# Performance work log

Hardware: AMD Instinct MI355X
Metric: run time of the kernel (lower is better)

## Reference

```python
import jax, jax.numpy as jnp
import numpy as np

H = 16          # num_heads
DK = 64         # k_dim_head
DV = 64         # v_dim_head
DIM = 1024      # model dim (= H*DK = H*DV)


def _split_heads(x, h):
    # ... T (H d) -> ... H T d
    x = x.reshape(x.shape[:-1] + (h, -1))
    return jnp.swapaxes(x, -2, -3)


def _merge_heads(x):
    # ... H T d -> ... T (H d)
    x = jnp.swapaxes(x, -2, -3)
    return x.reshape(x.shape[:-2] + (-1,))


def setup_inputs() -> dict:
    key = jax.random.key(0)
    ks = jax.random.split(key, 8)
    B, T = 2, 2048
    q = jax.random.normal(ks[0], (B, T, DIM), dtype=jnp.float32)
    k = jax.random.normal(ks[1], (B, T, DIM), dtype=jnp.float32)
    v = jax.random.normal(ks[2], (B, T, DIM), dtype=jnp.float32)
    # causal boolean mask [T, T] (True = attend)
    mask = jnp.tril(jnp.ones((T, T), dtype=bool))
    s = 1.0 / np.sqrt(DIM)
    # weights stored as [in, out] so projection is x @ W (== torch Linear, no bias)
    Wq = jax.random.normal(ks[3], (DIM, H * DK), dtype=jnp.float32) * s
    Wk = jax.random.normal(ks[4], (DIM, H * DK), dtype=jnp.float32) * s
    Wv = jax.random.normal(ks[5], (DIM, H * DV), dtype=jnp.float32) * s
    Wo = jax.random.normal(ks[6], (H * DV, DIM), dtype=jnp.float32) * s
    return {"q": q, "k": k, "v": v, "mask": mask,
            "Wq": Wq, "Wk": Wk, "Wv": Wv, "Wo": Wo}


def reference(q, k, v, mask, Wq, Wk, Wv, Wo):
    q_i = _split_heads(q @ Wq, H)                       # ... H T dk
    k_i = _split_heads(k @ Wk, H)                       # ... H T dk
    v_i = _split_heads(v @ Wv, H)                       # ... H T dv
    s_qk = jnp.einsum('...hik,...hjk->...hij', q_i, k_i) / jnp.sqrt(
        jnp.asarray(DK, dtype=q_i.dtype))               # ... H T T
    neg = -jnp.finfo(s_qk.dtype).max
    s_qk = jnp.where(mask, s_qk, neg)
    attn = jax.nn.softmax(s_qk, axis=-1)
    vals = jnp.einsum('...hij,...hjv->...hiv', attn, v_i)
    return _merge_heads(vals) @ Wo                      # ... T out_dim
```

## Files before the change

kernel.cpp:

```cpp
#include <hip/hip_runtime.h>
#include <hip/hip_bf16.h>
#include <stdint.h>

#define T_SEQ  2048
#define DMODEL 1024
#define NBATCH 2
#define NHEAD  16
#define DHEAD  64
#define MTOT   (NBATCH * T_SEQ)

typedef __attribute__((ext_vector_type(8))) short short8_t;
typedef __attribute__((ext_vector_type(4))) float f32x4;
typedef __attribute__((ext_vector_type(16))) float f32x16;
typedef __attribute__((ext_vector_type(2))) __bf16 bhalf2_t;
typedef __attribute__((ext_vector_type(4))) uint32_t uint4_t;

typedef const __attribute__((address_space(1))) void* gas_t;
typedef __attribute__((address_space(3))) void* las_t;

__device__ __forceinline__ ushort f2bf(float f) {
    return __builtin_bit_cast(unsigned short, (__bf16)f);
}
__device__ __forceinline__ uint32_t pk_bf16(float a, float b) {
    bhalf2_t t; t[0] = (__bf16)a; t[1] = (__bf16)b;
    return __builtin_bit_cast(uint32_t, t);
}

template <int B>
__device__ __forceinline__ short8_t pack8(const f32x16 &s) {
    uint4_t u;
    u[0] = pk_bf16(s[B + 0], s[B + 1]);
    u[1] = pk_bf16(s[B + 2], s[B + 3]);
    u[2] = pk_bf16(s[B + 4], s[B + 5]);
    u[3] = pk_bf16(s[B + 6], s[B + 7]);
    return __builtin_bit_cast(short8_t, u);
}

__global__ __launch_bounds__(256) void convert_qkv_kernel(
        const float* __restrict__ q, const float* __restrict__ k,
        const float* __restrict__ v, ushort* __restrict__ outb) {
    const size_t per = (size_t)MTOT * DMODEL / 4;
    size_t idx = (size_t)blockIdx.x * 256 + threadIdx.x;
    int t = (int)(idx / per);
    size_t i = idx - (size_t)t * per;
    const float4* src = (const float4*)(t == 0 ? q : (t == 1 ? k : v));
    float4 val = src[i];
    uint2 o;
    o.x = pk_bf16(val.x, val.y);
    o.y = pk_bf16(val.z, val.w);
    ((uint2*)outb)[(size_t)t * per + i] = o;
}

__global__ __launch_bounds__(256) void convw_kernel(
        const float* __restrict__ Wq, const float* __restrict__ Wk,
        const float* __restrict__ Wv, const float* __restrict__ Wo,
        ushort* __restrict__ wt) {
    __shared__ float tile[32][33];
    int z = blockIdx.z;
    const float* W = z == 0 ? Wq : z == 1 ? Wk : z == 2 ? Wv : Wo;
    const float sc = (z == 0) ? 0.18033688011f : 1.0f;
    ushort* out = wt + (size_t)z * DMODEL * DMODEL;
    int tx = threadIdx.x, ty = threadIdx.y;
    int k0 = blockIdx.x * 32, n0 = blockIdx.y * 32;
    #pragma unroll
    for (int i = 0; i < 4; i++)
        tile[ty + i * 8][tx] = W[(size_t)(k0 + ty + i * 8) * DMODEL + n0 + tx];
    __syncthreads();
    #pragma unroll
    for (int i = 0; i < 4; i++)
        out[(size_t)(n0 + ty + i * 8) * DMODEL + k0 + tx] = f2bf(tile[tx][ty + i * 8] * sc);
}

template <bool OUT_F32>
__global__ __launch_bounds__(256, 2) void gemm_bt_kernel(
        const ushort* __restrict__ Aall, const ushort* __restrict__ Btall,
        void* __restrict__ Call, int M, int N, int K) {
    const ushort* A  = Aall  + (size_t)blockIdx.z * M * K;
    const ushort* Bt = Btall + (size_t)blockIdx.z * N * K;

    __shared__ ushort As[128 * 32];
    __shared__ ushort Bs[128 * 32];

    const int tid  = threadIdx.x;
    const int lane = tid & 63;
    const int wid  = tid >> 6;
    const int wr = wid >> 1, wc = wid & 1;
    const int m_base = blockIdx.x * 128;
    const int n_base = blockIdx.y * 128;

    f32x4 acc[4][4] = {};

    const int srow = lane >> 2;
    const int scol = (lane & 3) * 8;

    for (int kk = 0; kk < K; kk += 32) {
        __syncthreads();
        #pragma unroll
        for (int i = 0; i < 2; i++) {
            int c = wid * 2 + i;
            const ushort* ga = A  + (size_t)(m_base + c * 16 + srow) * K + kk + scol;
            const ushort* gb = Bt + (size_t)(n_base + c * 16 + srow) * K + kk + scol;
            __builtin_amdgcn_global_load_lds((gas_t)ga, (las_t)(As + c * 512), 16, 0, 0);
            __builtin_amdgcn_global_load_lds((gas_t)gb, (las_t)(Bs + c * 512), 16, 0, 0);
        }
        __syncthreads();
        short8_t a[4], b[4];
        #pragma unroll
        for (int mt = 0; mt < 4; mt++)
            a[mt] = *(const short8_t*)(As + (wr * 64 + mt * 16 + (lane & 15)) * 32 + (lane >> 4) * 8);
        #pragma unroll
        for (int nt = 0; nt < 4; nt++)
            b[nt] = *(const short8_t*)(Bs + (wc * 64 + nt * 16 + (lane & 15)) * 32 + (lane >> 4) * 8);
        #pragma unroll
        for (int mt = 0; mt < 4; mt++)
            #pragma unroll
            for (int nt = 0; nt < 4; nt++)
                acc[mt][nt] = __builtin_amdgcn_mfma_f32_16x16x32_bf16(a[mt], b[nt], acc[mt][nt], 0, 0, 0);
    }

    const int row0 = m_base + wr * 64 + (lane >> 4) * 4;
    const int col0 = n_base + wc * 64 + (lane & 15);
    if constexpr (OUT_F32) {
        float* C = (float*)Call + (size_t)blockIdx.z * M * N;
        #pragma unroll
        for (int mt = 0; mt < 4; mt++)
            #pragma unroll
            for (int nt = 0; nt < 4; nt++)
                #pragma unroll
                for (int r = 0; r < 4; r++)
                    C[(size_t)(row0 + mt * 16 + r) * N + col0 + nt * 16] = acc[mt][nt][r];
    } else {
        ushort* C = (ushort*)Call + (size_t)blockIdx.z * M * N;
        #pragma unroll
        for (int mt = 0; mt < 4; mt++)
            #pragma unroll
            for (int nt = 0; nt < 4; nt++)
                #pragma unroll
                for (int r = 0; r < 4; r++)
                    C[(size_t)(row0 + mt * 16 + r) * N + col0 + nt * 16] = f2bf(acc[mt][nt][r]);
    }
}

__global__ __launch_bounds__(128, 2) void attn_kernel(
        const ushort* __restrict__ Qp, const ushort* __restrict__ Kp,
        const ushort* __restrict__ Vp, ushort* __restrict__ Op) {
    __shared__ __attribute__((aligned(16))) ushort Ksh[2][64 * 72];
    __shared__ __attribute__((aligned(16))) ushort Vts[2][64 * 72];

    const int tid = threadIdx.x, lane = tid & 63, w = tid >> 6;
    const int m31 = lane & 31, hi = lane >> 5;
    const int bh = blockIdx.y;
    const int b = bh >> 4, h = bh & 15;

    const ushort* Qb = Qp + (size_t)(b * T_SEQ) * DMODEL + h * DHEAD;
    const ushort* Kb = Kp + (size_t)(b * T_SEQ) * DMODEL + h * DHEAD;
    const ushort* Vb = Vp + (size_t)(b * T_SEQ) * DMODEL + h * DHEAD;
    ushort* Ob = Op + (size_t)(b * T_SEQ) * DMODEL + h * DHEAD;

    const int qi = 31 - (int)blockIdx.x;
    const int nt = qi + 1;
    const int q0 = qi * 64;
    const int q0w = q0 + w * 32;
    const int qg = q0w + m31;

    const int kr = tid >> 1, kc64 = (tid & 1) * 32;
    const int kvp = tid & 31, dvs = tid >> 5;
    const int lp = kvp & 7, q2 = lp >> 1;
    const int q2p = ((q2 & 1) << 1) | (q2 >> 1);
    const int kvc = (kvp & ~7) | (q2p << 1) | (lp & 1);

    short8_t kreg[4], vreg[4];
    auto LOADKV = [&](int kv0) {
        #pragma unroll
        for (int j = 0; j < 4; j++)
            kreg[j] = *(const short8_t*)(Kb + (size_t)(kv0 + kr) * DMODEL + kc64 + j * 8);
        const ushort* vsrc = Vb + (size_t)(kv0 + kvp * 2) * DMODEL + dvs * 16;
        vreg[0] = *(const short8_t*)(vsrc);
        vreg[1] = *(const short8_t*)(vsrc + 8);
        vreg[2] = *(const short8_t*)(vsrc + DMODEL);
        vreg[3] = *(const short8_t*)(vsrc + DMODEL + 8);
    };
    auto WRITEKV = [&](int buf) {
        #pragma unroll
        for (int j = 0; j < 4; j++)
            *(short8_t*)(&Ksh[buf][kr * 72 + kc64 + j * 8]) = kreg[j];
        #pragma unroll
        for (int c = 0; c < 2; c++) {
            uint4_t a = __builtin_bit_cast(uint4_t, vreg[c]);
            uint4_t o = __builtin_bit_cast(uint4_t, vreg[2 + c]);
            #pragma unroll
            for (int j = 0; j < 4; j++) {
                int d0 = dvs * 16 + c * 8 + 2 * j;
                *(uint32_t*)(&Vts[buf][(d0 + 0) * 72 + kvc * 2]) =
                    __builtin_amdgcn_perm(o[j], a[j], 0x05040100u);
                *(uint32_t*)(&Vts[buf][(d0 + 1) * 72 + kvc * 2]) =
                    __builtin_amdgcn_perm(o[j], a[j], 0x07060302u);
            }
        }
    };

    short8_t qf[4];
    #pragma unroll
    for (int dkc = 0; dkc < 4; dkc++)
        qf[dkc] = *(const short8_t*)(Qb + (size_t)(q0w + m31) * DMODEL + dkc * 16 + hi * 8);

    f32x16 acc0 = {}, acc1 = {};
    float mrun = -1e30f, lrun = 0.f;

    LOADKV(0);
    WRITEKV(0);
    LOADKV(64);

    for (int t = 0; t < nt; ++t) {
        const int kv0 = t * 64;
        const int cur = t & 1;
        const bool need_mask = (t == nt - 1);

        __syncthreads();
        if (t + 1 < nt) {
            WRITEKV(cur ^ 1);
            if (t + 2 < nt) LOADKV((t + 2) * 64);
        }

        f32x16 s0 = {}, s1 = {};
        __builtin_amdgcn_s_setprio(1);
        #pragma unroll
        for (int dkc = 0; dkc < 4; dkc++) {
            short8_t kf0 = *(const short8_t*)(&Ksh[cur][(m31) * 72 + dkc * 16 + hi * 8]);
            short8_t kf1 = *(const short8_t*)(&Ksh[cur][(32 + m31) * 72 + dkc * 16 + hi * 8]);
            s0 = __builtin_amdgcn_mfma_f32_32x32x16_bf16(kf0, qf[dkc], s0, 0, 0, 0);
            s1 = __builtin_amdgcn_mfma_f32_32x32x16_bf16(kf1, qf[dkc], s1, 0, 0, 0);
        }
        __builtin_amdgcn_s_setprio(0);

        if (need_mask) {
            const int kvb = kv0 + 4 * hi;
            #pragma unroll
            for (int r = 0; r < 16; r++) {
                int kvl = (r & 3) + 8 * (r >> 2);
                if (kvb + kvl      > qg) s0[r] = -1e30f;
                if (kvb + kvl + 32 > qg) s1[r] = -1e30f;
            }
        }

        float tm[16];
        #pragma unroll
        for (int r = 0; r < 16; r++) tm[r] = fmaxf(s0[r], s1[r]);
        #pragma unroll
        for (int st = 8; st >= 1; st >>= 1)
            #pragma unroll
            for (int i = 0; i < st; i++) tm[i] = fmaxf(tm[i], tm[i + st]);
        float pmax = fmaxf(tm[0], __shfl_xor(tm[0], 32));

        if (!__all(pmax <= mrun + 8.f)) {
            float mnew = fmaxf(mrun, pmax);
            float fac = exp2f(mrun - mnew);
            mrun = mnew;
            lrun *= fac;
            #pragma unroll
            for (int r = 0; r < 16; r++) {
                float fr = __shfl(fac, (r & 3) + 8 * (r >> 2) + 4 * hi);
                acc0[r] *= fr; acc1[r] *= fr;
            }
        }

        float ps[16];
        #pragma unroll
        for (int r = 0; r < 16; r++) {
            s0[r] = exp2f(s0[r] - mrun);
            s1[r] = exp2f(s1[r] - mrun);
            ps[r] = s0[r] + s1[r];
        }
        #pragma unroll
        for (int st = 8; st >= 1; st >>= 1)
            #pragma unroll
            for (int i = 0; i < st; i++) ps[i] += ps[i + st];
        lrun += ps[0] + __shfl_xor(ps[0], 32);

        short8_t pa[4];
        pa[0] = pack8<0>(s0);
        pa[1] = pack8<8>(s0);
        pa[2] = pack8<0>(s1);
        pa[3] = pack8<8>(s1);
        __builtin_amdgcn_s_setprio(1);
        #pragma unroll
        for (int ks = 0; ks < 4; ks++) {
            short8_t vf0 = *(const short8_t*)(&Vts[cur][(m31) * 72 + ks * 16 + hi * 8]);
            short8_t vf1 = *(const short8_t*)(&Vts[cur][(32 + m31) * 72 + ks * 16 + hi * 8]);
            acc0 = __builtin_amdgcn_mfma_f32_32x32x16_bf16(pa[ks], vf0, acc0, 0, 0, 0);
            acc1 = __builtin_amdgcn_mfma_f32_32x32x16_bf16(pa[ks], vf1, acc1, 0, 0, 0);
        }
        __builtin_amdgcn_s_setprio(0);
    }

    float linv = __builtin_amdgcn_rcpf(lrun);
    #pragma unroll
    for (int r = 0; r < 16; r++) {
        int ql = (r & 3) + 8 * (r >> 2) + 4 * hi;
        float li = __shfl(linv, ql);
        ushort* orow = Ob + (size_t)(q0w + ql) * DMODEL + m31;
        orow[0]  = f2bf(acc0[r] * li);
        orow[32] = f2bf(acc1[r] * li);
    }
}

extern "C" void kernel_launch(void* const* d_in, const int* in_sizes, int n_in,
                              void* d_out, int out_size, void* d_ws, size_t ws_size,
                              hipStream_t stream) {
    (void)in_sizes; (void)n_in; (void)out_size; (void)ws_size;
    const float* q  = (const float*)d_in[0];
    const float* k  = (const float*)d_in[1];
    const float* v  = (const float*)d_in[2];
    const float* Wq = (const float*)d_in[4];
    const float* Wk = (const float*)d_in[5];
    const float* Wv = (const float*)d_in[6];
    const float* Wo = (const float*)d_in[7];

    ushort* ws = (ushort*)d_ws;
    const size_t MK = (size_t)MTOT * DMODEL;
    const size_t NK = (size_t)DMODEL * DMODEL;
    ushort* qkvb = ws;
    ushort* wt   = ws + 3 * MK;
    ushort* qkvp = ws + 3 * MK + 4 * NK;
    ushort* Op   = ws;

    convert_qkv_kernel<<<dim3(12288), dim3(256), 0, stream>>>(q, k, v, qkvb);
    convw_kernel<<<dim3(32, 32, 4), dim3(32, 8), 0, stream>>>(Wq, Wk, Wv, Wo, wt);
    gemm_bt_kernel<false><<<dim3(32, 8, 3), dim3(256), 0, stream>>>(qkvb, wt, (void*)qkvp,
                                                                    MTOT, DMODEL, DMODEL);
    attn_kernel<<<dim3(32, 32), dim3(128), 0, stream>>>(qkvp, qkvp + MK, qkvp + 2 * MK, Op);
    gemm_bt_kernel<true><<<dim3(32, 8, 1), dim3(256), 0, stream>>>(Op, wt + 3 * NK, d_out,
                                                                   MTOT, DMODEL, DMODEL);
}
```

Before: 149.2 us.

## Schedule attention work units through a global atomic counter

The attention kernel now pulls work items from a global atomic counter, ordered longest-first (largest causal query tile first), instead of taking them from the fixed blockIdx mapping. A small kernel zeroes the counter before each launch. The aim is to balance the triangular causal workload across CUs so short tiles fill in behind long ones. The cost is an extra kernel launch plus two block barriers and an atomic per unit. The order also depends on the workspace having room for the counter.

New measurement: 149.3 us. Within noise of the previous version (+0.1%).

```diff
diff --git a/kernel.cpp b/kernel.cpp
--- a/kernel.cpp
+++ b/kernel.cpp
@@ -71,6 +71,10 @@
         out[(size_t)(n0 + ty + i * 8) * DMODEL + k0 + tx] = f2bf(tile[tx][ty + i * 8] * sc);
 }
 
+__global__ void zero_ctr_kernel(uint32_t* ctr) {
+    if (threadIdx.x == 0 && blockIdx.x == 0) *ctr = 0u;
+}
+
 template <bool OUT_F32>
 __global__ __launch_bounds__(256, 2) void gemm_bt_kernel(
         const ushort* __restrict__ Aall, const ushort* __restrict__ Btall,
@@ -143,25 +147,14 @@
 
 __global__ __launch_bounds__(128, 2) void attn_kernel(
         const ushort* __restrict__ Qp, const ushort* __restrict__ Kp,
-        const ushort* __restrict__ Vp, ushort* __restrict__ Op) {
+        const ushort* __restrict__ Vp, ushort* __restrict__ Op,
+        uint32_t* __restrict__ ctr) {
     __shared__ __attribute__((aligned(16))) ushort Ksh[2][64 * 72];
     __shared__ __attribute__((aligned(16))) ushort Vts[2][64 * 72];
+    __shared__ int unit_j;
 
     const int tid = threadIdx.x, lane = tid & 63, w = tid >> 6;
     const int m31 = lane & 31, hi = lane >> 5;
-    const int bh = blockIdx.y;
-    const int b = bh >> 4, h = bh & 15;
-
-    const ushort* Qb = Qp + (size_t)(b * T_SEQ) * DMODEL + h * DHEAD;
-    const ushort* Kb = Kp + (size_t)(b * T_SEQ) * DMODEL + h * DHEAD;
-    const ushort* Vb = Vp + (size_t)(b * T_SEQ) * DMODEL + h * DHEAD;
-    ushort* Ob = Op + (size_t)(b * T_SEQ) * DMODEL + h * DHEAD;
-
-    const int qi = 31 - (int)blockIdx.x;
-    const int nt = qi + 1;
-    const int q0 = qi * 64;
-    const int q0w = q0 + w * 32;
-    const int qg = q0w + m31;
 
     const int kr = tid >> 1, kc64 = (tid & 1) * 32;
     const int kvp = tid & 31, dvs = tid >> 5;
@@ -169,6 +162,8 @@
     const int q2p = ((q2 & 1) << 1) | (q2 >> 1);
     const int kvc = (kvp & ~7) | (q2p << 1) | (lp & 1);
 
+    const ushort *Qb, *Kb, *Vb;
+    ushort *Ob;
     short8_t kreg[4], vreg[4];
     auto LOADKV = [&](int kv0) {
         #pragma unroll
@@ -199,108 +194,128 @@
         }
     };
 
-    short8_t qf[4];
-    #pragma unroll
-    for (int dkc = 0; dkc < 4; dkc++)
-        qf[dkc] = *(const short8_t*)(Qb + (size_t)(q0w + m31) * DMODEL + dkc * 16 + hi * 8);
-
-    f32x16 acc0 = {}, acc1 = {};
-    float mrun = -1e30f, lrun = 0.f;
-
-    LOADKV(0);
-    WRITEKV(0);
-    LOADKV(64);
-
-    for (int t = 0; t < nt; ++t) {
-        const int kv0 = t * 64;
-        const int cur = t & 1;
-        const bool need_mask = (t == nt - 1);
-
+    for (;;) {
         __syncthreads();
-        if (t + 1 < nt) {
-            WRITEKV(cur ^ 1);
-            if (t + 2 < nt) LOADKV((t + 2) * 64);
+        if (tid == 0) unit_j = (int)atomicAdd(ctr, 1u);
+        __syncthreads();
+        const int j = unit_j;
+        if (j >= 1024) break;
+
+        const int u = 31 - (j >> 5);
+        const int bh = j & 31;
+        const int b = bh >> 4, h = bh & 15;
+        Qb = Qp + (size_t)(b * T_SEQ) * DMODEL + h * DHEAD;
+        Kb = Kp + (size_t)(b * T_SEQ) * DMODEL + h * DHEAD;
+        Vb = Vp + (size_t)(b * T_SEQ) * DMODEL + h * DHEAD;
+        Ob = Op + (size_t)(b * T_SEQ) * DMODEL + h * DHEAD;
+
+        const int nt = u + 1;
+        const int q0w = u * 64 + w * 32;
+        const int qg = q0w + m31;
+        const int diag = 2 * u + w;
+
+        short8_t qf[4];
+        #pragma unroll
+        for (int dkc = 0; dkc < 4; dkc++)
+            qf[dkc] = *(const short8_t*)(Qb + (size_t)(q0w + m31) * DMODEL + dkc * 16 + hi * 8);
+
+        f32x16 acc0 = {}, acc1 = {};
+        float mrun = -1e30f, lrun = 0.f;
+
+        LOADKV(0);
+        WRITEKV(0);
+        LOADKV(64);
+
+        for (int t = 0; t < nt; ++t) {
+            const int kv0 = t * 64;
+            const int cur = t & 1;
+            const bool need_mask = (t == nt - 1);
+
+            __syncthreads();
+            if (t + 1 < nt) {
+                WRITEKV(cur ^ 1);
+                if (t + 2 < nt) LOADKV((t + 2) * 64);
+            }
+
+            f32x16 s0 = {}, s1 = {};
+            __builtin_amdgcn_s_setprio(1);
+            #pragma unroll
+            for (int dkc = 0; dkc < 4; dkc++) {
+                short8_t kf0 = *(const short8_t*)(&Ksh[cur][(m31) * 72 + dkc * 16 + hi * 8]);
+                short8_t kf1 = *(const short8_t*)(&Ksh[cur][(32 + m31) * 72 + dkc * 16 + hi * 8]);
+                s0 = __builtin_amdgcn_mfma_f32_32x32x16_bf16(kf0, qf[dkc], s0, 0, 0, 0);
+                s1 = __builtin_amdgcn_mfma_f32_32x32x16_bf16(kf1, qf[dkc], s1, 0, 0, 0);
+            }
+            __builtin_amdgcn_s_setprio(0);
+
+            if (need_mask) {
+                const int kvb = kv0 + 4 * hi;
+                #pragma unroll
+                for (int r = 0; r < 16; r++) {
+                    int kvl = (r & 3) + 8 * (r >> 2);
+                    if (kvb + kvl      > qg) s0[r] = -1e30f;
+                    if (kvb + kvl + 32 > qg) s1[r] = -1e30f;
+                }
+            }
+
+            float tm[16];
+            #pragma unroll
+            for (int r = 0; r < 16; r++) tm[r] = fmaxf(s0[r], s1[r]);
+            #pragma unroll
+            for (int st = 8; st >= 1; st >>= 1)
+                #pragma unroll
+                for (int i = 0; i < st; i++) tm[i] = fmaxf(tm[i], tm[i + st]);
+            float pmax = fmaxf(tm[0], __shfl_xor(tm[0], 32));
+
+            if (!__all(pmax <= mrun + 8.f)) {
+                float mnew = fmaxf(mrun, pmax);
+                float fac = exp2f(mrun - mnew);
+                mrun = mnew;
+                lrun *= fac;
+                #pragma unroll
+                for (int r = 0; r < 16; r++) {
+                    float fr = __shfl(fac, (r & 3) + 8 * (r >> 2) + 4 * hi);
+                    acc0[r] *= fr; acc1[r] *= fr;
+                }
+            }
+            float ps[16];
+            #pragma unroll
+            for (int r = 0; r < 16; r++) {
+                s0[r] = exp2f(s0[r] - mrun);
+                s1[r] = exp2f(s1[r] - mrun);
+                ps[r] = s0[r] + s1[r];
+            }
+            #pragma unroll
+            for (int st = 8; st >= 1; st >>= 1)
+                #pragma unroll
+                for (int i = 0; i < st; i++) ps[i] += ps[i + st];
+            lrun += ps[0] + __shfl_xor(ps[0], 32);
+
+            short8_t pa[4];
+            pa[0] = pack8<0>(s0);
+            pa[1] = pack8<8>(s0);
+            pa[2] = pack8<0>(s1);
+            pa[3] = pack8<8>(s1);
+            __builtin_amdgcn_s_setprio(1);
+            #pragma unroll
+            for (int ks = 0; ks < 4; ks++) {
+                short8_t vf0 = *(const short8_t*)(&Vts[cur][(m31) * 72 + ks * 16 + hi * 8]);
+                short8_t vf1 = *(const short8_t*)(&Vts[cur][(32 + m31) * 72 + ks * 16 + hi * 8]);
+                acc0 = __builtin_amdgcn_mfma_f32_32x32x16_bf16(pa[ks], vf0, acc0, 0, 0, 0);
+                acc1 = __builtin_amdgcn_mfma_f32_32x32x16_bf16(pa[ks], vf1, acc1, 0, 0, 0);
+            }
+            __builtin_amdgcn_s_setprio(0);
         }
 
-        f32x16 s0 = {}, s1 = {};
-        __builtin_amdgcn_s_setprio(1);
-        #pragma unroll
-        for (int dkc = 0; dkc < 4; dkc++) {
-            short8_t kf0 = *(const short8_t*)(&Ksh[cur][(m31) * 72 + dkc * 16 + hi * 8]);
-            short8_t kf1 = *(const short8_t*)(&Ksh[cur][(32 + m31) * 72 + dkc * 16 + hi * 8]);
-            s0 = __builtin_amdgcn_mfma_f32_32x32x16_bf16(kf0, qf[dkc], s0, 0, 0, 0);
-            s1 = __builtin_amdgcn_mfma_f32_32x32x16_bf16(kf1, qf[dkc], s1, 0, 0, 0);
+        float linv = __builtin_amdgcn_rcpf(lrun);
+        #pragma unroll
+        for (int r = 0; r < 16; r++) {
+            int ql = (r & 3) + 8 * (r >> 2) + 4 * hi;
+            float li = __shfl(linv, ql);
+            ushort* orow = Ob + (size_t)(q0w + ql) * DMODEL + m31;
+            orow[0]  = f2bf(acc0[r] * li);
+            orow[32] = f2bf(acc1[r] * li);
         }
-        __builtin_amdgcn_s_setprio(0);
-
-        if (need_mask) {
-            const int kvb = kv0 + 4 * hi;
-            #pragma unroll
-            for (int r = 0; r < 16; r++) {
-                int kvl = (r & 3) + 8 * (r >> 2);
-                if (kvb + kvl      > qg) s0[r] = -1e30f;
-                if (kvb + kvl + 32 > qg) s1[r] = -1e30f;
-            }
-        }
-
-        float tm[16];
-        #pragma unroll
-        for (int r = 0; r < 16; r++) tm[r] = fmaxf(s0[r], s1[r]);
-        #pragma unroll
-        for (int st = 8; st >= 1; st >>= 1)
-            #pragma unroll
-            for (int i = 0; i < st; i++) tm[i] = fmaxf(tm[i], tm[i + st]);
-        float pmax = fmaxf(tm[0], __shfl_xor(tm[0], 32));
-
-        if (!__all(pmax <= mrun + 8.f)) {
-            float mnew = fmaxf(mrun, pmax);
-            float fac = exp2f(mrun - mnew);
-            mrun = mnew;
-            lrun *= fac;
-            #pragma unroll
-            for (int r = 0; r < 16; r++) {
-                float fr = __shfl(fac, (r & 3) + 8 * (r >> 2) + 4 * hi);
-                acc0[r] *= fr; acc1[r] *= fr;
-            }
-        }
-
-        float ps[16];
-        #pragma unroll
-        for (int r = 0; r < 16; r++) {
-            s0[r] = exp2f(s0[r] - mrun);
-            s1[r] = exp2f(s1[r] - mrun);
-            ps[r] = s0[r] + s1[r];
-        }
-        #pragma unroll
-        for (int st = 8; st >= 1; st >>= 1)
-            #pragma unroll
-            for (int i = 0; i < st; i++) ps[i] += ps[i + st];
-        lrun += ps[0] + __shfl_xor(ps[0], 32);
-
-        short8_t pa[4];
-        pa[0] = pack8<0>(s0);
-        pa[1] = pack8<8>(s0);
-        pa[2] = pack8<0>(s1);
-        pa[3] = pack8<8>(s1);
-        __builtin_amdgcn_s_setprio(1);
-        #pragma unroll
-        for (int ks = 0; ks < 4; ks++) {
-            short8_t vf0 = *(const short8_t*)(&Vts[cur][(m31) * 72 + ks * 16 + hi * 8]);
-            short8_t vf1 = *(const short8_t*)(&Vts[cur][(32 + m31) * 72 + ks * 16 + hi * 8]);
-            acc0 = __builtin_amdgcn_mfma_f32_32x32x16_bf16(pa[ks], vf0, acc0, 0, 0, 0);
-            acc1 = __builtin_amdgcn_mfma_f32_32x32x16_bf16(pa[ks], vf1, acc1, 0, 0, 0);
-        }
-        __builtin_amdgcn_s_setprio(0);
-    }
-
-    float linv = __builtin_amdgcn_rcpf(lrun);
-    #pragma unroll
-    for (int r = 0; r < 16; r++) {
-        int ql = (r & 3) + 8 * (r >> 2) + 4 * hi;
-        float li = __shfl(linv, ql);
-        ushort* orow = Ob + (size_t)(q0w + ql) * DMODEL + m31;
-        orow[0]  = f2bf(acc0[r] * li);
-        orow[32] = f2bf(acc1[r] * li);
     }
 }
 
@@ -323,12 +338,14 @@
     ushort* wt   = ws + 3 * MK;
     ushort* qkvp = ws + 3 * MK + 4 * NK;
     ushort* Op   = ws;
+    uint32_t* ctr = (uint32_t*)(ws + 3 * MK + 4 * NK + 3 * MK);
 
     convert_qkv_kernel<<<dim3(12288), dim3(256), 0, stream>>>(q, k, v, qkvb);
     convw_kernel<<<dim3(32, 32, 4), dim3(32, 8), 0, stream>>>(Wq, Wk, Wv, Wo, wt);
+    zero_ctr_kernel<<<dim3(1), dim3(64), 0, stream>>>(ctr);
     gemm_bt_kernel<false><<<dim3(32, 8, 3), dim3(256), 0, stream>>>(qkvb, wt, (void*)qkvp,
                                                                     MTOT, DMODEL, DMODEL);
-    attn_kernel<<<dim3(32, 32), dim3(128), 0, stream>>>(qkvp, qkvp + MK, qkvp + 2 * MK, Op);
+    attn_kernel<<<dim3(1024), dim3(128), 0, stream>>>(qkvp, qkvp + MK, qkvp + 2 * MK, Op, ctr);
     gemm_bt_kernel<true><<<dim3(32, 8, 1), dim3(256), 0, stream>>>(Op, wt + 3 * NK, d_out,
                                                                    MTOT, DMODEL, DMODEL);
 }
```
